# Kernel tuning notes

Hardware: AMD Instinct MI355X
Metric: run time of the kernel (lower is better)

Reference implementation:

```python
import jax, jax.numpy as jnp
import numpy as np

E = 768      # embed_size
H = 12       # num_heads inside each nn.MultiheadAttention
G = 4        # num_groups
D = E // H   # per-head dim = 64


def setup_inputs() -> dict:
    key = jax.random.key(0)
    ks = jax.random.split(key, 20)
    s = 0.02
    B, S = 2, 2048
    inp = {
        "query": jax.random.normal(ks[0], (B, S, E), jnp.float32),
        "key":   jax.random.normal(ks[1], (B, S, E), jnp.float32),
        "value": jax.random.normal(ks[2], (B, S, E), jnp.float32),
        # outer projections (query_group_proj / key_proj / value_proj)
        "Wqg": jax.random.normal(ks[3], (E, E), jnp.float32) * s,
        "bqg": jnp.zeros((E,), jnp.float32),
        "Wk":  jax.random.normal(ks[4], (E, E), jnp.float32) * s,
        "bk":  jnp.zeros((E,), jnp.float32),
        "Wv":  jax.random.normal(ks[5], (E, E), jnp.float32) * s,
        "bv":  jnp.zeros((E,), jnp.float32),
        # per-group MultiheadAttention params (in_proj split into q/k/v, out_proj)
        "Wq_in": jax.random.normal(ks[6], (G, E, E), jnp.float32) * s,
        "bq_in": jnp.zeros((G, E), jnp.float32),
        "Wk_in": jax.random.normal(ks[7], (G, E, E), jnp.float32) * s,
        "bk_in": jnp.zeros((G, E), jnp.float32),
        "Wv_in": jax.random.normal(ks[8], (G, E, E), jnp.float32) * s,
        "bv_in": jnp.zeros((G, E), jnp.float32),
        "Wout":  jax.random.normal(ks[9], (G, E, E), jnp.float32) * s,
        "bout":  jnp.zeros((G, E), jnp.float32),
    }
    return inp


def reference(query, key, value, Wqg, bqg, Wk, bk, Wv, bv,
              Wq_in, bq_in, Wk_in, bk_in, Wv_in, bv_in, Wout, bout):
    B, S, _ = query.shape
    T = S // G  # tokens per group
    scale = 1.0 / np.sqrt(D).astype(np.float32)

    # outer projections (Linear: x @ W.T + b)
    q = query @ Wqg.T + bqg                         # [B,S,E]
    k = key   @ Wk.T  + bk                          # [B,S,E]
    v = value @ Wv.T  + bv                          # [B,S,E]

    # split query tokens into G interleaved groups (view + permute in source)
    qg = q.reshape(B, T, G, E).transpose(0, 2, 1, 3)  # [B,G,T,E]

    # per-group MHA input projections (batched over groups)
    qi = jnp.einsum('bgte,gfe->bgtf', qg, Wq_in) + bq_in[None, :, None, :]
    ki = jnp.einsum('bse,gfe->bgsf', k,  Wk_in) + bk_in[None, :, None, :]
    vi = jnp.einsum('bse,gfe->bgsf', v,  Wv_in) + bv_in[None, :, None, :]

    qh = qi.reshape(B, G, T, H, D)
    kh = ki.reshape(B, G, S, H, D)
    vh = vi.reshape(B, G, S, H, D)

    scores = jnp.einsum('bgthd,bgshd->bghts', qh, kh) * scale  # [B,G,H,T,S]
    attn = jax.nn.softmax(scores, axis=-1)
    ctx = jnp.einsum('bghts,bgshd->bgthd', attn, vh).reshape(B, G, T, E)

    out_g = jnp.einsum('bgte,gfe->bgtf', ctx, Wout) + bout[None, :, None, :]  # [B,G,T,E]

    # reassemble sequence order (inverse of the grouping permutation)
    out = out_g.transpose(0, 2, 1, 3).reshape(B, S, E)
    return out
```

## Files before the change

### kernel.cpp

```cpp
#include <hip/hip_runtime.h>
#include <hip/hip_bf16.h>


typedef __attribute__((ext_vector_type(8))) short short8;
typedef __attribute__((ext_vector_type(4))) float floatx4;
typedef __attribute__((ext_vector_type(4))) int intx4;

static __device__ __forceinline__ short f2bf(float f) {
    __bf16 b = (__bf16)f;
    return __builtin_bit_cast(short, b);
}
static __device__ __forceinline__ short8 f8_to_bf8(floatx4 f0, floatx4 f1) {
    short8 s;
    s[0]=f2bf(f0[0]); s[1]=f2bf(f0[1]); s[2]=f2bf(f0[2]); s[3]=f2bf(f0[3]);
    s[4]=f2bf(f1[0]); s[5]=f2bf(f1[1]); s[6]=f2bf(f1[2]); s[7]=f2bf(f1[3]);
    return s;
}
static __device__ __forceinline__ unsigned cvt_pk_bf16(float a, float b) {
    unsigned r;
    asm("v_cvt_pk_bf16_f32 %0, %1, %2" : "=v"(r) : "v"(a), "v"(b));
    return r;
}
static __device__ __forceinline__ void gload_lds16(const short* g, short* l) {
    __builtin_amdgcn_global_load_lds(
        (const __attribute__((address_space(1))) unsigned int*)g,
        (__attribute__((address_space(3))) unsigned int*)l, 16, 0, 0);
}

__global__ __launch_bounds__(256) void cast_w(
    const float* a0, const float* a1, const float* a2, const float* a3,
    const float* a4, const float* a5, const float* a6, short* dst)
{
    const long U = 589824L;
    const float* ptrs[7] = {a0,a1,a2,a3,a4,a5,a6};
    const long starts[8] = {0, U, 2*U, 3*U, 7*U, 11*U, 15*U, 19*U};
    long i = (long)blockIdx.x * 2048 + (long)threadIdx.x * 8;
    int t = 0;
    while (t < 6 && i >= starts[t + 1]) t++;
    const float* s = ptrs[t] + (i - starts[t]);
    floatx4 f0 = *(const floatx4*)s;
    floatx4 f1 = *(const floatx4*)(s + 4);
    *(short8*)(dst + i) = f8_to_bf8(f0, f1);
}

#define GEMM_LANE_VARS                                                        \
    const int tid = threadIdx.x, lane = tid & 63, w = tid >> 6;               \
    const int wm = w & 1, wn = w >> 1;                                        \
    const int qr = lane >> 4, lc = lane & 15, x7 = lc & 7;                    \
    const int srow = tid >> 3, schunk = tid & 7, sx = srow & 7;

template<int CMODE, int BIAS_MODE>
static __device__ __forceinline__ void gemm_epilogue(
    floatx4 (&acc)[4][4], const float* bp, void* Cv, int ldc, int bm, int bn,
    int wm, int wn, int qr, int lc)
{
#pragma unroll
    for (int ni = 0; ni < 4; ni++) {
        const int gcol = bn * 128 + wn * 64 + ni * 16 + lc;
        const float bcol = (BIAS_MODE == 0) ? bp[gcol] : 0.f;
#pragma unroll
        for (int mi = 0; mi < 4; mi++) {
#pragma unroll
            for (int r = 0; r < 4; r++) {
                const int grow = bm * 128 + wm * 64 + mi * 16 + qr * 4 + r;
                const float bb = (BIAS_MODE == 1) ? bp[grow] : bcol;
                const float v = acc[mi][ni][r] + bb;
                if (CMODE == 0)
                    ((short*)Cv)[(long)grow * ldc + gcol] = f2bf(v);
                else
                    ((float*)Cv)[(long)grow * ldc + gcol] = v;
            }
        }
    }
}

static __device__ __forceinline__ void gemm_mfma_step(
    floatx4 (&acc)[4][4], const short* Ac, const short* Bc,
    int wm, int wn, int qr, int lc, int x7)
{
#pragma unroll
    for (int ks = 0; ks < 64; ks += 32) {
        const int c0 = (ks >> 3) + qr;
        const int slot = ((c0 ^ x7) << 3);
        short8 af[4], bfr[4];
#pragma unroll
        for (int mi = 0; mi < 4; mi++)
            af[mi] = *(const short8*)&Ac[(wm * 64 + mi * 16 + lc) * 64 + slot];
#pragma unroll
        for (int ni = 0; ni < 4; ni++)
            bfr[ni] = *(const short8*)&Bc[(wn * 64 + ni * 16 + lc) * 64 + slot];
#pragma unroll
        for (int mi = 0; mi < 4; mi++)
#pragma unroll
            for (int ni = 0; ni < 4; ni++)
                acc[mi][ni] = __builtin_amdgcn_mfma_f32_16x16x32_bf16(
                    af[mi], bfr[ni], acc[mi][ni], 0, 0, 0);
    }
}

template<int CMODE, int BIAS_MODE>
static __device__ __forceinline__ void gemm_core_db(
    const short* __restrict__ A, const short* __restrict__ Wb,
    const float* __restrict__ bp, void* __restrict__ Cv,
    int lda, int ldc, int bm, int bn, short* As, short* Bs)
{
    GEMM_LANE_VARS
    const short* Ab = A + (long)(bm * 128) * lda;
    const short* Wt = Wb + (long)(bn * 128) * 768;
    const int gch = ((schunk ^ sx) << 3);

    floatx4 acc[4][4];
#pragma unroll
    for (int mi = 0; mi < 4; mi++)
#pragma unroll
        for (int ni = 0; ni < 4; ni++) acc[mi][ni] = (floatx4){0.f, 0.f, 0.f, 0.f};

#pragma unroll
    for (int p = 0; p < 4; p++) {
        gload_lds16(Ab + (long)(p * 32 + srow) * lda + gch, &As[(p * 32 + w * 8) * 64]);
        gload_lds16(Wt + (long)(p * 32 + srow) * 768 + gch, &Bs[(p * 32 + w * 8) * 64]);
    }

    for (int kk = 0; kk < 12; kk++) {
        __syncthreads();
        if (kk < 11) {
            const int k1 = (kk + 1) * 64;
            const int nb = ((kk + 1) & 1) * 8192;
#pragma unroll
            for (int p = 0; p < 4; p++) {
                gload_lds16(Ab + (long)(p * 32 + srow) * lda + k1 + gch,
                            &As[nb + (p * 32 + w * 8) * 64]);
                gload_lds16(Wt + (long)(p * 32 + srow) * 768 + k1 + gch,
                            &Bs[nb + (p * 32 + w * 8) * 64]);
            }
        }
        gemm_mfma_step(acc, As + (kk & 1) * 8192, Bs + (kk & 1) * 8192,
                       wm, wn, qr, lc, x7);
    }
    gemm_epilogue<CMODE, BIAS_MODE>(acc, bp, Cv, ldc, bm, bn, wm, wn, qr, lc);
}

template<int CMODE, int BIAS_MODE>
static __device__ __forceinline__ void gemm_core_f32(
    const float* __restrict__ A, const short* __restrict__ Wb,
    const float* __restrict__ bp, void* __restrict__ Cv,
    int lda, int ldc, int bm, int bn, short* As, short* Bs)
{
    GEMM_LANE_VARS
    const short* Wt = Wb + (long)(bn * 128) * 768;

    floatx4 acc[4][4];
#pragma unroll
    for (int mi = 0; mi < 4; mi++)
#pragma unroll
        for (int ni = 0; ni < 4; ni++) acc[mi][ni] = (floatx4){0.f, 0.f, 0.f, 0.f};

    for (int k0 = 0; k0 < 768; k0 += 64) {
        __syncthreads();
#pragma unroll
        for (int p = 0; p < 4; p++) {
            const int row = p * 32 + srow;
            const float* ap = A + (long)(bm * 128 + row) * lda + k0 + schunk * 8;
            floatx4 f0 = *(const floatx4*)ap;
            floatx4 f1 = *(const floatx4*)(ap + 4);
            *(short8*)&As[row * 64 + ((schunk ^ sx) << 3)] = f8_to_bf8(f0, f1);
            gload_lds16(Wt + (long)row * 768 + k0 + ((schunk ^ sx) << 3),
                        &Bs[(p * 32 + w * 8) * 64]);
        }
        __syncthreads();
        gemm_mfma_step(acc, As, Bs, wm, wn, qr, lc, x7);
    }
    gemm_epilogue<CMODE, BIAS_MODE>(acc, bp, Cv, ldc, bm, bn, wm, wn, qr, lc);
}

__global__ __launch_bounds__(256) void qkv_gemm(
    const float* q, const float* k, const float* v, const short* Wbf,
    const float* bq, const float* bk, const float* bv, short* outp)
{
    __shared__ short As[128 * 64];
    __shared__ short Bs[128 * 64];
    const int xcd = blockIdx.x & 7, slot = blockIdx.x >> 3;
    const int bm = xcd * 4 + slot / 18;
    const int rem = slot % 18, y = rem / 6, bn = rem % 6;
    const float* A    = (y == 0) ? q  : (y == 1) ? k  : v;
    const float* bias = (y == 0) ? bq : (y == 1) ? bk : bv;
    gemm_core_f32<0, 0>(A, Wbf + (long)y * 589824, bias, outp + (long)y * 3145728,
                        768, 768, bm, bn, As, Bs);
}

template<int BIAS_MODE>
static __device__ __forceinline__ void gemm256_core(
    const short* __restrict__ A, const short* __restrict__ B,
    const float* __restrict__ bias, short* __restrict__ C,
    int lda, int ldc, int bm, int bn, short* As, short* Bs)
{
    const int tid = threadIdx.x, lane = tid & 63, w = tid >> 6;
    const int wm = w & 1, wn = w >> 1;
    const int qr = lane >> 4, lc = lane & 15, x7 = lc & 7;
    const int srow = tid >> 3, schunk = tid & 7;
    const int gch = ((schunk ^ (srow & 7)) << 3);

    const short* Ab = A + (long)(bm * 256) * lda;
    const short* Bb = B + (long)(bn * 256) * 768;

    floatx4 acc[8][4];
#pragma unroll
    for (int i = 0; i < 8; i++)
#pragma unroll
        for (int j = 0; j < 4; j++) acc[i][j] = (floatx4){0.f, 0.f, 0.f, 0.f};

#pragma unroll
    for (int r = 0; r < 256; r += 64) {
        gload_lds16(Ab + (long)(r + srow) * lda + gch, As + (r + w * 8) * 64);
        gload_lds16(Bb + (long)(r + srow) * 768 + gch, Bs + (r + w * 8) * 64);
    }

#pragma unroll 1
    for (int kt = 0; kt < 12; ++kt) {
        const int s = kt & 1;
        const short* Ac = As + s * 16384;
        const short* Bc = Bs + s * 16384;
        short* Ad = As + (1 - s) * 16384;
        short* Bd = Bs + (1 - s) * 16384;
        const int koff = (kt + 1) * 64;

        asm volatile("s_waitcnt vmcnt(0)" ::: "memory");
        __builtin_amdgcn_s_barrier();

        short8 af[4][2], bfr[2][2];
#pragma unroll
        for (int ph = 0; ph < 4; ++ph) {
            const int mh = ph >> 1, nh = ph & 1;
            if (nh == 0) {
#pragma unroll
                for (int mi = 0; mi < 4; mi++)
#pragma unroll
                    for (int ks = 0; ks < 2; ks++)
                        af[mi][ks] = *(const short8*)&Ac[
                            (wm * 128 + (mh * 4 + mi) * 16 + lc) * 64 +
                            ((((ks << 2) + qr) ^ x7) << 3)];
            }
#pragma unroll
            for (int ni = 0; ni < 2; ni++)
#pragma unroll
                for (int ks = 0; ks < 2; ks++)
                    bfr[ni][ks] = *(const short8*)&Bc[
                        (wn * 64 + (nh * 2 + ni) * 16 + lc) * 64 +
                        ((((ks << 2) + qr) ^ x7) << 3)];
            if (kt < 11) {
                const int r = ph * 64;
                gload_lds16(Ab + (long)(r + srow) * lda + koff + gch,
                            Ad + (r + w * 8) * 64);
                gload_lds16(Bb + (long)(r + srow) * 768 + koff + gch,
                            Bd + (r + w * 8) * 64);
            }
            __builtin_amdgcn_s_barrier();
            asm volatile("s_waitcnt lgkmcnt(0)" ::: "memory");
            __builtin_amdgcn_sched_barrier(0);
            __builtin_amdgcn_s_setprio(1);
#pragma unroll
            for (int ks = 0; ks < 2; ks++)
#pragma unroll
                for (int mi = 0; mi < 4; mi++)
#pragma unroll
                    for (int ni = 0; ni < 2; ni++)
                        acc[mh * 4 + mi][nh * 2 + ni] =
                            __builtin_amdgcn_mfma_f32_16x16x32_bf16(
                                af[mi][ks], bfr[ni][ks],
                                acc[mh * 4 + mi][nh * 2 + ni], 0, 0, 0);
            __builtin_amdgcn_s_setprio(0);
            __builtin_amdgcn_sched_barrier(0);
            __builtin_amdgcn_s_barrier();
        }
    }

#pragma unroll
    for (int ni = 0; ni < 4; ni++) {
        const int gcol = bn * 256 + wn * 64 + ni * 16 + lc;
        const float bcol = (BIAS_MODE == 0) ? bias[gcol] : 0.f;
#pragma unroll
        for (int mi = 0; mi < 8; mi++) {
#pragma unroll
            for (int r = 0; r < 4; r++) {
                const int grow = bm * 256 + wm * 128 + mi * 16 + qr * 4 + r;
                const float bb = (BIAS_MODE == 1) ? bias[grow] : bcol;
                C[(long)grow * ldc + gcol] = f2bf(acc[mi][ni][r] + bb);
            }
        }
    }
}

__global__ __launch_bounds__(512, 2) void mid_gemm2(
    const short* kproj, const short* vproj, const short* qproj, const short* Wbf,
    const float* bq_in, const float* bk_in, const float* bv_in,
    short* kiB, short* vtB, short* qiB)
{
    __shared__ short As[2 * 16384];
    __shared__ short Bs[2 * 16384];
    const int xcd = blockIdx.x & 7, slot = blockIdx.x >> 3;
    const int z = xcd, b = z >> 2, g = z & 3;
    if (slot < 24) {
        gemm256_core<0>(kproj + (long)b * 1572864, Wbf + (long)(7 + g) * 589824,
                        bk_in + g * 768, kiB + (long)z * 1572864,
                        768, 768, slot / 3, slot % 3, As, Bs);
    } else if (slot < 48) {
        const int s2 = slot - 24;
        gemm256_core<1>(Wbf + (long)(11 + g) * 589824, vproj + (long)b * 1572864,
                        bv_in + g * 768, vtB + (long)z * 1572864,
                        768, 2048, s2 / 8, s2 % 8, As, Bs);
    } else {
        const int s3 = slot - 48;
        gemm256_core<0>(qproj + (long)b * 1572864 + g * 768, Wbf + (long)(3 + g) * 589824,
                        bq_in + g * 768, qiB + (long)z * 393216,
                        3072, 768, s3 / 3, s3 % 3, As, Bs);
    }
}

__global__ __launch_bounds__(256) void out_gemm(
    const short* ctxB, const short* Wbf, const float* bout, float* out)
{
    extern __shared__ short sm[];
    short* As = sm;
    short* Bs = sm + 16384;
    const int xcd = blockIdx.x & 7, slot = blockIdx.x >> 3;
    const int z = xcd, b = z >> 2, g = z & 3;
    gemm_core_db<2, 0>(ctxB + (long)z * 393216, Wbf + (long)(15 + g) * 589824,
                       bout + g * 768, out + (long)b * 1572864 + g * 768,
                       768, 3072, slot / 6, slot % 6, As, Bs);
}

__global__ __launch_bounds__(256) void attn_kernel(
    const short* __restrict__ qi, const short* __restrict__ ki,
    const short* __restrict__ vt, short* __restrict__ ctx)
{
    __shared__ short Kt[2][64 * 64];
    __shared__ short Vt[2][64 * 64];

    const int tid = threadIdx.x, lane = tid & 63, w = tid >> 6;
    const int qr = lane >> 4, lc = lane & 15, x7 = lc & 7;
    const int headid = blockIdx.x % 96;
    const int tile = blockIdx.x / 96;
    const int h = headid % 12, bg = headid / 12;

    const short* qp = qi + ((long)bg * 512 + tile * 64 + w * 16 + lc) * 768 + h * 64 + qr * 8;
    const short8 aq0 = *(const short8*)qp;
    const short8 aq1 = *(const short8*)(qp + 32);

    floatx4 cacc[4];
    float lsum = 0.f;
#pragma unroll
    for (int dc = 0; dc < 4; dc++) cacc[dc] = (floatx4){0.f, 0.f, 0.f, 0.f};

    const int srow = lane >> 3, schk = lane & 7, swz = schk ^ srow;
    const short* kgb = ki + ((long)bg * 2048) * 768 + h * 64;
    const short* vgb = vt + ((long)(bg * 768 + h * 64)) * 2048;

#define KPERM(d) ((((d) >> 5) & 1) * 32 + (((d) >> 2) & 3) * 8 + (((d) >> 4) & 1) * 4 + ((d) & 3))
    const int d0 = w * 16 + srow, d1 = d0 + 8;
    const int kp0 = KPERM(d0), kp1 = KPERM(d1);
#undef KPERM

    {
        gload_lds16(kgb + (long)kp0 * 768 + swz * 8, &Kt[0][(w * 16) * 64]);
        gload_lds16(kgb + (long)kp1 * 768 + swz * 8, &Kt[0][(w * 16 + 8) * 64]);
        gload_lds16(vgb + (long)d0 * 2048 + swz * 8, &Vt[0][(w * 16) * 64]);
        gload_lds16(vgb + (long)d1 * 2048 + swz * 8, &Vt[0][(w * 16 + 8) * 64]);
    }

    for (int it = 0; it < 32; it++) {
        const int cur = it & 1;
        __syncthreads();
        if (it < 31) {
            const int nxt = cur ^ 1, s0 = (it + 1) * 64;
            gload_lds16(kgb + (long)(s0 + kp0) * 768 + swz * 8, &Kt[nxt][(w * 16) * 64]);
            gload_lds16(kgb + (long)(s0 + kp1) * 768 + swz * 8, &Kt[nxt][(w * 16 + 8) * 64]);
            gload_lds16(vgb + (long)d0 * 2048 + s0 + swz * 8, &Vt[nxt][(w * 16) * 64]);
            gload_lds16(vgb + (long)d1 * 2048 + s0 + swz * 8, &Vt[nxt][(w * 16 + 8) * 64]);
        }

        const short* Kb = &Kt[cur][0];
        const short* Vb = &Vt[cur][0];

        floatx4 sv[4];
        __builtin_amdgcn_s_setprio(1);
#pragma unroll
        for (int ss = 0; ss < 4; ss++) {
            const short* kr = Kb + (ss * 16 + lc) * 64;
            short8 b0 = *(const short8*)(kr + ((qr ^ x7) << 3));
            short8 b1 = *(const short8*)(kr + (((4 + qr) ^ x7) << 3));
            floatx4 t = (floatx4){0.f, 0.f, 0.f, 0.f};
            t = __builtin_amdgcn_mfma_f32_16x16x32_bf16(b0, aq0, t, 0, 0, 0);
            t = __builtin_amdgcn_mfma_f32_16x16x32_bf16(b1, aq1, t, 0, 0, 0);
            sv[ss] = t;
        }
        __builtin_amdgcn_s_setprio(0);

        float p[4][4];
#pragma unroll
        for (int ss = 0; ss < 4; ss++)
#pragma unroll
            for (int r = 0; r < 4; r++)
                p[ss][r] = __builtin_amdgcn_exp2f(sv[ss][r] * 0.18033688f);
#pragma unroll
        for (int ss = 0; ss < 4; ss++)
            lsum += (p[ss][0] + p[ss][1]) + (p[ss][2] + p[ss][3]);

        intx4 i0, i1;
        i0[0] = (int)cvt_pk_bf16(p[0][0], p[0][1]);
        i0[1] = (int)cvt_pk_bf16(p[0][2], p[0][3]);
        i0[2] = (int)cvt_pk_bf16(p[1][0], p[1][1]);
        i0[3] = (int)cvt_pk_bf16(p[1][2], p[1][3]);
        i1[0] = (int)cvt_pk_bf16(p[2][0], p[2][1]);
        i1[1] = (int)cvt_pk_bf16(p[2][2], p[2][3]);
        i1[2] = (int)cvt_pk_bf16(p[3][0], p[3][1]);
        i1[3] = (int)cvt_pk_bf16(p[3][2], p[3][3]);
        const short8 ap0 = __builtin_bit_cast(short8, i0);
        const short8 ap1 = __builtin_bit_cast(short8, i1);

        __builtin_amdgcn_s_setprio(1);
#pragma unroll
        for (int dc = 0; dc < 4; dc++) {
            const short* vr = Vb + (dc * 16 + lc) * 64;
            short8 bv0 = *(const short8*)(vr + ((qr ^ x7) << 3));
            short8 bv1 = *(const short8*)(vr + (((4 + qr) ^ x7) << 3));
            cacc[dc] = __builtin_amdgcn_mfma_f32_16x16x32_bf16(ap0, bv0, cacc[dc], 0, 0, 0);
            cacc[dc] = __builtin_amdgcn_mfma_f32_16x16x32_bf16(ap1, bv1, cacc[dc], 0, 0, 0);
        }
        __builtin_amdgcn_s_setprio(0);
    }

    lsum += __shfl_xor(lsum, 16);
    lsum += __shfl_xor(lsum, 32);
    float linv[4];
#pragma unroll
    for (int r = 0; r < 4; r++)
        linv[r] = 1.f / __shfl(lsum, qr * 4 + r);

    short* cp = ctx + ((long)bg * 512 + tile * 64 + w * 16) * 768 + h * 64;
#pragma unroll
    for (int dc = 0; dc < 4; dc++)
#pragma unroll
        for (int r = 0; r < 4; r++)
            cp[(qr * 4 + r) * 768 + dc * 16 + lc] = f2bf(cacc[dc][r] * linv[r]);
}

extern "C" void kernel_launch(void* const* d_in, const int* in_sizes, int n_in,
                              void* d_out, int out_size, void* d_ws, size_t ws_size,
                              hipStream_t stream) {
    const float* query = (const float*)d_in[0];
    const float* key   = (const float*)d_in[1];
    const float* value = (const float*)d_in[2];
    const float* Wqg = (const float*)d_in[3];  const float* bqg = (const float*)d_in[4];
    const float* Wk  = (const float*)d_in[5];  const float* bk  = (const float*)d_in[6];
    const float* Wv  = (const float*)d_in[7];  const float* bv  = (const float*)d_in[8];
    const float* Wq_in = (const float*)d_in[9];  const float* bq_in = (const float*)d_in[10];
    const float* Wk_in = (const float*)d_in[11]; const float* bk_in = (const float*)d_in[12];
    const float* Wv_in = (const float*)d_in[13]; const float* bv_in = (const float*)d_in[14];
    const float* Wout  = (const float*)d_in[15]; const float* bout  = (const float*)d_in[16];
    float* out = (float*)d_out;

    short* ws     = (short*)d_ws;
    short* Wbf    = ws;
    short* q_proj = ws + 11206656L;
    short* k_proj = ws + 14352384L;
    short* v_proj = ws + 17498112L;
    short* qiB    = ws + 20643840L;
    short* vtB    = ws + 23789568L;
    short* kiB    = ws + 36372480L;
    short* ctxB   = ws + 11206656L;

    dim3 blk(256);

    cast_w<<<dim3(5472), blk, 0, stream>>>(
        Wqg, Wk, Wv, Wq_in, Wk_in, Wv_in, Wout, Wbf);

    qkv_gemm<<<dim3(576), blk, 0, stream>>>(
        query, key, value, Wbf, bqg, bk, bv, q_proj);

    mid_gemm2<<<dim3(432), dim3(512), 0, stream>>>(
        k_proj, v_proj, q_proj, Wbf, bq_in, bk_in, bv_in, kiB, vtB, qiB);

    attn_kernel<<<dim3(768), blk, 0, stream>>>(qiB, kiB, vtB, ctxB);

    out_gemm<<<dim3(192), blk, 65536, stream>>>(ctxB, Wbf, bout, out);
}
```

Measured before the change: 289.8 us.

## Process two 16-row query tiles per wave in attention with 128-thread blocks

The attention kernel now uses two waves per block instead of four, with each wave handling 32 query rows (two 16-row MFMA tiles). Each K and V fragment read from LDS is reused for two MFMAs, which halves LDS read traffic per unit of compute. Each wave also issues twice as many global-to-LDS loads per tile. The trade-off is more registers per wave and fewer waves per block to hide latency behind the barrier and softmax exponentials.

```diff
diff --git a/kernel.cpp b/kernel.cpp
--- a/kernel.cpp
+++ b/kernel.cpp
@@ -329,7 +329,7 @@
                        768, 3072, slot / 6, slot % 6, As, Bs);
 }
 
-__global__ __launch_bounds__(256) void attn_kernel(
+__global__ __launch_bounds__(128) void attn_kernel(
     const short* __restrict__ qi, const short* __restrict__ ki,
     const short* __restrict__ vt, short* __restrict__ ctx)
 {
@@ -341,30 +341,44 @@
     const int headid = blockIdx.x % 96;
     const int tile = blockIdx.x / 96;
     const int h = headid % 12, bg = headid / 12;
-
-    const short* qp = qi + ((long)bg * 512 + tile * 64 + w * 16 + lc) * 768 + h * 64 + qr * 8;
-    const short8 aq0 = *(const short8*)qp;
-    const short8 aq1 = *(const short8*)(qp + 32);
-
-    floatx4 cacc[4];
-    float lsum = 0.f;
-#pragma unroll
-    for (int dc = 0; dc < 4; dc++) cacc[dc] = (floatx4){0.f, 0.f, 0.f, 0.f};
+    const long qrow0 = (long)bg * 512 + tile * 64 + w * 32;
+
+    short8 aq[2][2];
+#pragma unroll
+    for (int t = 0; t < 2; t++) {
+        const short* qp = qi + (qrow0 + t * 16 + lc) * 768 + h * 64 + qr * 8;
+        aq[t][0] = *(const short8*)qp;
+        aq[t][1] = *(const short8*)(qp + 32);
+    }
+
+    floatx4 cacc[2][4];
+    float lsum[2] = {0.f, 0.f};
+#pragma unroll
+    for (int t = 0; t < 2; t++)
+#pragma unroll
+        for (int dc = 0; dc < 4; dc++) cacc[t][dc] = (floatx4){0.f, 0.f, 0.f, 0.f};
 
     const int srow = lane >> 3, schk = lane & 7, swz = schk ^ srow;
     const short* kgb = ki + ((long)bg * 2048) * 768 + h * 64;
     const short* vgb = vt + ((long)(bg * 768 + h * 64)) * 2048;
 
 #define KPERM(d) ((((d) >> 5) & 1) * 32 + (((d) >> 2) & 3) * 8 + (((d) >> 4) & 1) * 4 + ((d) & 3))
-    const int d0 = w * 16 + srow, d1 = d0 + 8;
-    const int kp0 = KPERM(d0), kp1 = KPERM(d1);
+    int kp[4], dv[4];
+#pragma unroll
+    for (int inst = 0; inst < 4; inst++) {
+        dv[inst] = w * 32 + inst * 8 + srow;
+        kp[inst] = KPERM(dv[inst]);
+    }
 #undef KPERM
 
     {
-        gload_lds16(kgb + (long)kp0 * 768 + swz * 8, &Kt[0][(w * 16) * 64]);
-        gload_lds16(kgb + (long)kp1 * 768 + swz * 8, &Kt[0][(w * 16 + 8) * 64]);
-        gload_lds16(vgb + (long)d0 * 2048 + swz * 8, &Vt[0][(w * 16) * 64]);
-        gload_lds16(vgb + (long)d1 * 2048 + swz * 8, &Vt[0][(w * 16 + 8) * 64]);
+#pragma unroll
+        for (int inst = 0; inst < 4; inst++) {
+            gload_lds16(kgb + (long)kp[inst] * 768 + swz * 8,
+                        &Kt[0][(w * 32 + inst * 8) * 64]);
+            gload_lds16(vgb + (long)dv[inst] * 2048 + swz * 8,
+                        &Vt[0][(w * 32 + inst * 8) * 64]);
+        }
     }
 
     for (int it = 0; it < 32; it++) {
@@ -372,50 +386,59 @@
         __syncthreads();
         if (it < 31) {
             const int nxt = cur ^ 1, s0 = (it + 1) * 64;
-            gload_lds16(kgb + (long)(s0 + kp0) * 768 + swz * 8, &Kt[nxt][(w * 16) * 64]);
-            gload_lds16(kgb + (long)(s0 + kp1) * 768 + swz * 8, &Kt[nxt][(w * 16 + 8) * 64]);
-            gload_lds16(vgb + (long)d0 * 2048 + s0 + swz * 8, &Vt[nxt][(w * 16) * 64]);
-            gload_lds16(vgb + (long)d1 * 2048 + s0 + swz * 8, &Vt[nxt][(w * 16 + 8) * 64]);
+#pragma unroll
+            for (int inst = 0; inst < 4; inst++) {
+                gload_lds16(kgb + (long)(s0 + kp[inst]) * 768 + swz * 8,
+                            &Kt[nxt][(w * 32 + inst * 8) * 64]);
+                gload_lds16(vgb + (long)dv[inst] * 2048 + s0 + swz * 8,
+                            &Vt[nxt][(w * 32 + inst * 8) * 64]);
+            }
         }
 
         const short* Kb = &Kt[cur][0];
         const short* Vb = &Vt[cur][0];
 
-        floatx4 sv[4];
+        floatx4 sv[2][4];
         __builtin_amdgcn_s_setprio(1);
 #pragma unroll
         for (int ss = 0; ss < 4; ss++) {
             const short* kr = Kb + (ss * 16 + lc) * 64;
             short8 b0 = *(const short8*)(kr + ((qr ^ x7) << 3));
             short8 b1 = *(const short8*)(kr + (((4 + qr) ^ x7) << 3));
-            floatx4 t = (floatx4){0.f, 0.f, 0.f, 0.f};
-            t = __builtin_amdgcn_mfma_f32_16x16x32_bf16(b0, aq0, t, 0, 0, 0);
-            t = __builtin_amdgcn_mfma_f32_16x16x32_bf16(b1, aq1, t, 0, 0, 0);
-            sv[ss] = t;
+#pragma unroll
+            for (int t = 0; t < 2; t++) {
+                floatx4 acc0 = (floatx4){0.f, 0.f, 0.f, 0.f};
+                acc0 = __builtin_amdgcn_mfma_f32_16x16x32_bf16(b0, aq[t][0], acc0, 0, 0, 0);
+                acc0 = __builtin_amdgcn_mfma_f32_16x16x32_bf16(b1, aq[t][1], acc0, 0, 0, 0);
+                sv[t][ss] = acc0;
+            }
         }
         __builtin_amdgcn_s_setprio(0);
 
-        float p[4][4];
-#pragma unroll
-        for (int ss = 0; ss < 4; ss++)
-#pragma unroll
-            for (int r = 0; r < 4; r++)
-                p[ss][r] = __builtin_amdgcn_exp2f(sv[ss][r] * 0.18033688f);
-#pragma unroll
-        for (int ss = 0; ss < 4; ss++)
-            lsum += (p[ss][0] + p[ss][1]) + (p[ss][2] + p[ss][3]);
-
-        intx4 i0, i1;
-        i0[0] = (int)cvt_pk_bf16(p[0][0], p[0][1]);
-        i0[1] = (int)cvt_pk_bf16(p[0][2], p[0][3]);
-        i0[2] = (int)cvt_pk_bf16(p[1][0], p[1][1]);
-        i0[3] = (int)cvt_pk_bf16(p[1][2], p[1][3]);
-        i1[0] = (int)cvt_pk_bf16(p[2][0], p[2][1]);
-        i1[1] = (int)cvt_pk_bf16(p[2][2], p[2][3]);
-        i1[2] = (int)cvt_pk_bf16(p[3][0], p[3][1]);
-        i1[3] = (int)cvt_pk_bf16(p[3][2], p[3][3]);
-        const short8 ap0 = __builtin_bit_cast(short8, i0);
-        const short8 ap1 = __builtin_bit_cast(short8, i1);
+        short8 ap[2][2];
+#pragma unroll
+        for (int t = 0; t < 2; t++) {
+            float p[4][4];
+#pragma unroll
+            for (int ss = 0; ss < 4; ss++)
+#pragma unroll
+                for (int r = 0; r < 4; r++)
+                    p[ss][r] = __builtin_amdgcn_exp2f(sv[t][ss][r] * 0.18033688f);
+#pragma unroll
+            for (int ss = 0; ss < 4; ss++)
+                lsum[t] += (p[ss][0] + p[ss][1]) + (p[ss][2] + p[ss][3]);
+            intx4 i0, i1;
+            i0[0] = (int)cvt_pk_bf16(p[0][0], p[0][1]);
+            i0[1] = (int)cvt_pk_bf16(p[0][2], p[0][3]);
+            i0[2] = (int)cvt_pk_bf16(p[1][0], p[1][1]);
+            i0[3] = (int)cvt_pk_bf16(p[1][2], p[1][3]);
+            i1[0] = (int)cvt_pk_bf16(p[2][0], p[2][1]);
+            i1[1] = (int)cvt_pk_bf16(p[2][2], p[2][3]);
+            i1[2] = (int)cvt_pk_bf16(p[3][0], p[3][1]);
+            i1[3] = (int)cvt_pk_bf16(p[3][2], p[3][3]);
+            ap[t][0] = __builtin_bit_cast(short8, i0);
+            ap[t][1] = __builtin_bit_cast(short8, i1);
+        }
 
         __builtin_amdgcn_s_setprio(1);
 #pragma unroll
@@ -423,25 +446,34 @@
             const short* vr = Vb + (dc * 16 + lc) * 64;
             short8 bv0 = *(const short8*)(vr + ((qr ^ x7) << 3));
             short8 bv1 = *(const short8*)(vr + (((4 + qr) ^ x7) << 3));
-            cacc[dc] = __builtin_amdgcn_mfma_f32_16x16x32_bf16(ap0, bv0, cacc[dc], 0, 0, 0);
-            cacc[dc] = __builtin_amdgcn_mfma_f32_16x16x32_bf16(ap1, bv1, cacc[dc], 0, 0, 0);
+#pragma unroll
+            for (int t = 0; t < 2; t++) {
+                cacc[t][dc] = __builtin_amdgcn_mfma_f32_16x16x32_bf16(
+                    ap[t][0], bv0, cacc[t][dc], 0, 0, 0);
+                cacc[t][dc] = __builtin_amdgcn_mfma_f32_16x16x32_bf16(
+                    ap[t][1], bv1, cacc[t][dc], 0, 0, 0);
+            }
         }
         __builtin_amdgcn_s_setprio(0);
     }
 
-    lsum += __shfl_xor(lsum, 16);
-    lsum += __shfl_xor(lsum, 32);
-    float linv[4];
-#pragma unroll
-    for (int r = 0; r < 4; r++)
-        linv[r] = 1.f / __shfl(lsum, qr * 4 + r);
-
-    short* cp = ctx + ((long)bg * 512 + tile * 64 + w * 16) * 768 + h * 64;
-#pragma unroll
-    for (int dc = 0; dc < 4; dc++)
-#pragma unroll
-        for (int r = 0; r < 4; r++)
-            cp[(qr * 4 + r) * 768 + dc * 16 + lc] = f2bf(cacc[dc][r] * linv[r]);
+#pragma unroll
+    for (int t = 0; t < 2; t++) {
+        lsum[t] += __shfl_xor(lsum[t], 16);
+        lsum[t] += __shfl_xor(lsum[t], 32);
+    }
+    short* cp = ctx + (qrow0)*768 + h * 64;
+#pragma unroll
+    for (int t = 0; t < 2; t++) {
+#pragma unroll
+        for (int r = 0; r < 4; r++) {
+            const float linv = 1.f / __shfl(lsum[t], qr * 4 + r);
+#pragma unroll
+            for (int dc = 0; dc < 4; dc++)
+                cp[(t * 16 + qr * 4 + r) * 768 + dc * 16 + lc] =
+                    f2bf(cacc[t][dc][r] * linv);
+        }
+    }
 }
 
 extern "C" void kernel_launch(void* const* d_in, const int* in_sizes, int n_in,
@@ -480,7 +512,7 @@
     mid_gemm2<<<dim3(432), dim3(512), 0, stream>>>(
         k_proj, v_proj, q_proj, Wbf, bq_in, bk_in, bv_in, kiB, vtB, qiB);
 
-    attn_kernel<<<dim3(768), blk, 0, stream>>>(qiB, kiB, vtB, ctxB);
+    attn_kernel<<<dim3(768), dim3(128), 0, stream>>>(qiB, kiB, vtB, ctxB);
 
     out_gemm<<<dim3(192), blk, 65536, stream>>>(ctxB, Wbf, bout, out);
 }
```

After: 303.0 us. +4.5%, slower.
